# Performance work log

Hardware: AMD Instinct MI355X
Metric: run time of the kernel (lower is better)

The kernel has to match this reference:

```python
import jax, jax.numpy as jnp
import numpy as np

PI = 3.141592653589793
DET_THRESHOLD = 0.25
MAX_DET = 100
REG_HEAD = 4
DEPTH_MEAN = 28.01  # smoke_coder.depth_ref[0]
DIM_REF = (3.88, 1.63, 1.53)  # smoke_coder.dim_ref[0] (l, h, w)


def setup_inputs() -> dict:
    key = jax.random.key(0)
    k1, k2, k3, k4 = jax.random.split(key, 4)
    B, C, H, W = 32, 3, 256, 832  # stride-4 feature map of 3328x1024 images
    pred_heatmap = jax.random.uniform(k1, (B, C, H, W), dtype=jnp.float32)
    pred_regression = jax.random.normal(k2, (B, C + 1, H, W), dtype=jnp.float32) * 0.1  # REG_HEAD=4 channels
    trans_mat = jnp.tile(jnp.array([[0.25, 0.0, 0.0], [0.0, 0.25, 0.0], [0.0, 0.0, 1.0]], jnp.float32), (B, 1, 1))
    K_mat = jnp.tile(jnp.array([[2100.0, 0.0, 1664.0], [0.0, 2100.0, 512.0], [0.0, 0.0, 1.0]], jnp.float32), (B, 1, 1))
    size = jnp.tile(jnp.array([3328.0, 1024.0], jnp.float32), (B, 1))  # (img_w, img_h)
    h_cam = jax.random.uniform(k3, (B,), jnp.float32, 1.4, 2.0)
    dimensions = jax.random.uniform(k4, (B, 3), jnp.float32, 1.5, 4.0)
    return dict(pred_heatmap=pred_heatmap, pred_regression=pred_regression, trans_mat=trans_mat,
                K_mat=K_mat, size=size, h_cam=h_cam, dimensions=dimensions)


def reference(pred_heatmap, pred_regression, trans_mat, K_mat, size, h_cam, dimensions):
    B, C, H, W = pred_heatmap.shape
    K = MAX_DET
    # ---- nms_hm: 3x3 max-pool, keep local maxima ----
    hmax = jax.lax.reduce_window(pred_heatmap, -jnp.inf, jax.lax.max, (1, 1, 3, 3), (1, 1, 1, 1), 'SAME')
    heat = pred_heatmap * (hmax == pred_heatmap).astype(pred_heatmap.dtype)
    # ---- select_topk: per-class topk then global topk ----
    scores_c, inds_c = jax.lax.top_k(heat.reshape(B, C, H * W), K)  # [B,C,K]
    ys_c = (inds_c // W).astype(jnp.float32)
    xs_c = (inds_c % W).astype(jnp.float32)
    scores, topk_ind = jax.lax.top_k(scores_c.reshape(B, C * K), K)  # [B,K]
    clses = (topk_ind // K).astype(jnp.float32)
    inds = jnp.take_along_axis(inds_c.reshape(B, C * K), topk_ind, axis=1)
    ys = jnp.take_along_axis(ys_c.reshape(B, C * K), topk_ind, axis=1)
    xs = jnp.take_along_axis(xs_c.reshape(B, C * K), topk_ind, axis=1)
    feat = pred_regression.reshape(B, REG_HEAD, H * W).transpose(0, 2, 1)  # [B,HW,R]
    pois = jnp.take_along_axis(feat, inds[:, :, None], axis=1).reshape(-1, REG_HEAD)  # [B*K,R]
    log_dv_delta = pois[:, 0]
    off_u = pois[:, 1]
    ori = pois[:, 2:]
    # ---- feature points -> image points via inverse affine ----
    pts = jnp.stack([xs.reshape(-1), ys.reshape(-1)], axis=1)
    pts = pts + jnp.stack([off_u, jnp.zeros_like(off_u)], axis=1)
    pts_h = jnp.concatenate([pts, jnp.ones((pts.shape[0], 1), pts.dtype)], axis=1)  # [N,3]
    obj = jnp.repeat(jnp.arange(B), K)
    trans_inv = jnp.linalg.inv(trans_mat)[obj]  # [N,3,3]
    img_pts = jnp.einsum('nij,nj->ni', trans_inv, pts_h)[:, :2]
    # ---- per-object camera params ----
    Ks = K_mat[obj]
    h = h_cam[obj]
    kd = dimensions[obj]
    fx, fy, cx = Ks[:, 0, 0], Ks[:, 1, 1], Ks[:, 0, 2]
    dim_ref = jnp.array(DIM_REF, jnp.float32)
    dims = jnp.where(jnp.isfinite(kd), kd, dim_ref[None, :])
    # ---- geometric depth decode ----
    h_ref = h - dims[:, 1] / 2.0
    log_dv_ref = jnp.log(jnp.clip(fy * jnp.abs(h_ref), 1e-7, None) / DEPTH_MEAN)
    log_dv = jnp.clip(log_dv_ref + log_dv_delta, -4.0, 8.0)
    depths = jnp.clip(fy * jnp.abs(h_ref) * jnp.exp(-log_dv), 0.5, 120.0)
    px = (img_pts[:, 0] - cx) * depths / fx
    locs = jnp.stack([px, h, depths], axis=1)  # [N,3]
    # ---- decode_orientation (SMOKE) ----
    rays = jnp.arctan(locs[:, 0] / (locs[:, 2] + 1e-7))
    alphas = jnp.arctan(ori[:, 0] / (ori[:, 1] + 1e-7))
    alphas = alphas + jnp.where(ori[:, 1] >= 0, -PI / 2, PI / 2)
    rotys = alphas + rays
    rotys = jnp.where(rotys > PI, rotys - 2 * PI, rotys)
    rotys = jnp.where(rotys < -PI, rotys + 2 * PI, rotys)
    # ---- encode_box2d: build 3D corners, rotate, project, clamp ----
    cos, sin = jnp.cos(rotys), jnp.sin(rotys)
    cx8 = jnp.array([-0.5, 0.5, 0.5, 0.5, 0.5, -0.5, -0.5, -0.5], jnp.float32)
    cy8 = jnp.array([-1.0, -1.0, 0.0, 0.0, -1.0, -1.0, 0.0, 0.0], jnp.float32)
    cz8 = jnp.array([-0.5, -0.5, -0.5, 0.5, 0.5, 0.5, 0.5, -0.5], jnp.float32)
    xc = dims[:, 0:1] * cx8  # l
    yc = dims[:, 1:2] * cy8  # h
    zc = dims[:, 2:3] * cz8  # w
    bx = cos[:, None] * xc + sin[:, None] * zc
    bz = -sin[:, None] * xc + cos[:, None] * zc
    box3d = jnp.stack([bx, yc, bz], axis=1) + locs[:, :, None]  # [N,3,8]
    proj = jnp.einsum('nij,njk->nik', Ks, box3d)
    uv = proj[:, :2, :] / proj[:, 2:3, :]
    img_w = size.reshape(-1)[0]
    img_h = size.reshape(-1)[1]
    xmins = jnp.clip(jnp.min(uv[:, 0, :], axis=1), 0.0, img_w)
    xmaxs = jnp.clip(jnp.max(uv[:, 0, :], axis=1), 0.0, img_w)
    ymins = jnp.clip(jnp.min(uv[:, 1, :], axis=1), 0.0, img_h)
    ymaxs = jnp.clip(jnp.max(uv[:, 1, :], axis=1), 0.0, img_h)
    box2d = jnp.stack([xmins, ymins, xmaxs, ymaxs], axis=1)
    pred_dims = jnp.roll(dims, -1, axis=1)  # (l,h,w)->(h,w,l)
    result = jnp.concatenate([clses.reshape(-1, 1), alphas[:, None], box2d, pred_dims, locs,
                              rotys[:, None], scores.reshape(-1, 1)], axis=1)  # [N,14]
    # fixed-shape equivalent of boolean filtering: zero out rows below threshold
    keep = (result[:, -1] > DET_THRESHOLD).astype(result.dtype)
    return result * keep[:, None]
```

## Files before the change

kernel.cpp:

```cpp
#include <hip/hip_runtime.h>
#include <math.h>

#define B_ 32
#define C_ 3
#define H_ 256
#define W_ 832
#define HW_ (H_*W_)
#define NQ (W_/4)
#define K_ 100
#define RPB 16
#define PARTS (H_/RPB)
#define BLK 256
#define CAP 2048
#define NB 2048
#define TIE_CAP 128
#define SEL_PASSES 6
#define QPW 62
#define SLOTS 384
#define T_HOT 0.982f
#define NCAND2 (C_*PARTS*SLOTS)

typedef unsigned long long ull;

template<int N>
__device__ inline void bitonic_sort_desc(ull* s) {
    for (int k = 2; k <= N; k <<= 1) {
        for (int j = k >> 1; j > 0; j >>= 1) {
            __syncthreads();
            for (int i = threadIdx.x; i < N; i += BLK) {
                int ixj = i ^ j;
                if (ixj > i) {
                    ull a = s[i], b = s[ixj];
                    bool up = ((i & k) == 0);
                    if (up ? (a < b) : (a > b)) { s[i] = b; s[ixj] = a; }
                }
            }
        }
    }
    __syncthreads();
}

__device__ inline void find_digit(const unsigned* __restrict__ hist,
                                  unsigned* __restrict__ wtot,
                                  const int kneed,
                                  int* __restrict__ d_s,
                                  int* __restrict__ krem_s,
                                  int* __restrict__ m_s) {
    const int tid = threadIdx.x;
    const int lane = tid & 63;
    const int wid = tid >> 6;
    unsigned l[8];
    unsigned Ls = 0;
    #pragma unroll
    for (int j = 0; j < 8; ++j) { l[j] = hist[tid * 8 + j]; Ls += l[j]; }
    unsigned x = Ls;
    #pragma unroll
    for (int off = 1; off < 64; off <<= 1) {
        unsigned y = __shfl_down(x, off);
        if (lane + off < 64) x += y;
    }
    if (lane == 0) wtot[wid] = x;
    __syncthreads();
    unsigned tail = 0;
    #pragma unroll
    for (int w = 0; w < 4; ++w) if (w > wid) tail += wtot[w];
    unsigned s = x - Ls + tail;
    #pragma unroll
    for (int j = 7; j >= 0; --j) {
        const unsigned Sj = s + l[j];
        if (Sj >= (unsigned)kneed && s < (unsigned)kneed) {
            *d_s = tid * 8 + j;
            *krem_s = kneed - (int)s;
            *m_s = (int)l[j];
        }
        s = Sj;
    }
    __syncthreads();
}

__device__ inline void select_topk(const ull* __restrict__ buf, const int cnt,
                                   ull* __restrict__ dst,
                                   unsigned* __restrict__ hist,
                                   ull* __restrict__ tie,
                                   unsigned* __restrict__ wtot,
                                   int* __restrict__ sh) {
    const int tid = threadIdx.x;
    const int lane = tid & 63;
    if (tid == 0) sh[0] = 0;
    int kneed = K_;
    int pshift = 0;
    ull prefix = 0;
    for (int pass = 0; pass < SEL_PASSES; ++pass) {
        const int rs = 53 - 11 * pass;
        const int shift = (rs > 0) ? rs : 0;
        #pragma unroll
        for (int j = 0; j < NB / BLK; ++j) hist[tid + j * BLK] = 0u;
        if (tid == 0) sh[1] = 0;
        __syncthreads();
        if (pass == 0) {
            for (int i = tid; i < cnt; i += BLK) {
                const unsigned dg = (unsigned)(buf[i] >> shift) & 2047u;
                ull unclaimed = __ballot(1);
                while (unclaimed) {
                    const int leader = __ffsll((long long)unclaimed) - 1;
                    const unsigned ldg = __shfl(dg, leader);
                    const ull same = __ballot(dg == ldg);
                    if (lane == leader)
                        atomicAdd(&hist[ldg], (unsigned)__popcll(same));
                    unclaimed &= ~same;
                }
            }
        } else {
            for (int i = tid; i < cnt; i += BLK) {
                const ull key = buf[i];
                if ((key >> pshift) != prefix) continue;
                atomicAdd(&hist[(unsigned)(key >> shift) & 2047u], 1u);
            }
        }
        __syncthreads();
        find_digit(hist, wtot, kneed, &sh[2], &sh[3], &sh[4]);
        const int d = sh[2], krem = sh[3], m = sh[4];
        const bool last = (m <= TIE_CAP) || (pass == SEL_PASSES - 1);
        for (int i = tid; i < cnt; i += BLK) {
            const ull key = buf[i];
            if (pass > 0 && (key >> pshift) != prefix) continue;
            const int dg = (int)((unsigned)(key >> shift) & 2047u);
            if (dg > d) {
                dst[atomicAdd(&sh[0], 1)] = key;
            } else if (last && dg == d) {
                const int p = atomicAdd(&sh[1], 1);
                if (p < TIE_CAP) tie[p] = key;
            }
        }
        __syncthreads();
        if (last) {
            const int n1 = K_ - krem;
            if (sh[1] <= TIE_CAP) {
                const int mm = sh[1];
                for (int i = tid; i < mm; i += BLK) {
                    const ull key = tie[i];
                    int r = 0;
                    for (int j = 0; j < mm; ++j) r += (tie[j] > key) ? 1 : 0;
                    if (r < krem) dst[n1 + r] = key;
                }
            } else {
                for (int i = tid; i < krem; i += BLK) dst[n1 + i] = tie[0];
            }
            __syncthreads();
            return;
        }
        prefix = (prefix << 11) | (ull)(unsigned)d;
        pshift = shift;
        kneed = krem;
    }
}

__device__ inline void select_topk_g(const ull* __restrict__ A, const int cnt,
                                     ull* __restrict__ dst,
                                     unsigned* __restrict__ hist,
                                     ull* __restrict__ tie,
                                     unsigned* __restrict__ wtot,
                                     int* __restrict__ sh) {
    const int tid = threadIdx.x;
    const int lane = tid & 63;
    if (tid == 0) sh[0] = 0;
    int kneed = K_;
    int pshift = 0;
    ull prefix = 0;
    for (int pass = 0; pass < SEL_PASSES; ++pass) {
        const int rs = 53 - 11 * pass;
        const int shift = (rs > 0) ? rs : 0;
        #pragma unroll
        for (int j = 0; j < NB / BLK; ++j) hist[tid + j * BLK] = 0u;
        if (tid == 0) sh[1] = 0;
        __syncthreads();
        if (pass == 0) {
            for (int i = tid; i < cnt; i += BLK) {
                const unsigned dg = (unsigned)(A[i] >> shift) & 2047u;
                ull unclaimed = __ballot(1);
                while (unclaimed) {
                    const int leader = __ffsll((long long)unclaimed) - 1;
                    const unsigned ldg = __shfl(dg, leader);
                    const ull same = __ballot(dg == ldg);
                    if (lane == leader)
                        atomicAdd(&hist[ldg], (unsigned)__popcll(same));
                    unclaimed &= ~same;
                }
            }
        } else {
            for (int i = tid; i < cnt; i += BLK) {
                const ull key = A[i];
                if ((key >> pshift) != prefix) continue;
                atomicAdd(&hist[(unsigned)(key >> shift) & 2047u], 1u);
            }
        }
        __syncthreads();
        find_digit(hist, wtot, kneed, &sh[2], &sh[3], &sh[4]);
        const int d = sh[2], krem = sh[3], m = sh[4];
        const bool last = (m <= TIE_CAP) || (pass == SEL_PASSES - 1);
        for (int i = tid; i < cnt; i += BLK) {
            const ull key = A[i];
            if (pass > 0 && (key >> pshift) != prefix) continue;
            const int dg = (int)((unsigned)(key >> shift) & 2047u);
            if (dg > d) {
                dst[atomicAdd(&sh[0], 1)] = key;
            } else if (last && dg == d) {
                const int p = atomicAdd(&sh[1], 1);
                if (p < TIE_CAP) tie[p] = key;
            }
        }
        __syncthreads();
        if (last) {
            const int n1 = K_ - krem;
            if (sh[1] <= TIE_CAP) {
                const int mm = sh[1];
                for (int i = tid; i < mm; i += BLK) {
                    const ull key = tie[i];
                    int r = 0;
                    for (int j = 0; j < mm; ++j) r += (tie[j] > key) ? 1 : 0;
                    if (r < krem) dst[n1 + r] = key;
                }
            } else {
                for (int i = tid; i < krem; i += BLK) dst[n1 + i] = tie[0];
            }
            __syncthreads();
            return;
        }
        prefix = (prefix << 11) | (ull)(unsigned)d;
        pshift = shift;
        kneed = krem;
    }
}

__global__ void __launch_bounds__(BLK) topk_part_kernel(
        const float* __restrict__ heat, ull* __restrict__ parts2) {
    const int chan = blockIdx.x / PARTS;
    const int c    = chan % C_;
    const int part = blockIdx.x % PARTS;
    const float* __restrict__ hp = heat + (size_t)chan * HW_;
    const int r0 = part * RPB;
    const int tid = threadIdx.x;
    const int lane = tid & 63;
    const int wid = tid >> 6;

    const int q = QPW * wid + lane - 1;
    const bool ghost = (q < 0) || (q >= NQ);
    const int qc = (q < 0) ? 0 : ((q >= NQ) ? NQ - 1 : q);
    const bool emitter = (lane >= 1) && (lane <= QPW) && !ghost;

    __shared__ ull sbuf[CAP];
    __shared__ unsigned hist[NB];
    __shared__ ull tie[TIE_CAP];
    __shared__ unsigned wtot[4];
    __shared__ int scnt, nhot, wpos;
    __shared__ int selsh[5];
    if (tid == 0) { scnt = 0; nhot = 0; wpos = 0; }

    float4 R[6];
    #pragma unroll
    for (int j = 0; j < 6; ++j) {
        int row = r0 - 1 + j;
        row = (row < 0) ? 0 : ((row > H_ - 1) ? H_ - 1 : row);
        R[j] = reinterpret_cast<const float4*>(hp + (size_t)row * W_)[qc];
    }
    __syncthreads();

    #pragma unroll
    for (int r = 0; r < RPB; ++r) {
        const int y = r0 + r;
        const float4 ra = R[r % 6];
        const float4 rb = R[(r + 1) % 6];
        const float4 rc = R[(r + 2) % 6];
        if (r < RPB - 4) {
            const int yn = (y + 5 > H_ - 1) ? H_ - 1 : y + 5;
            R[r % 6] = reinterpret_cast<const float4*>(hp + (size_t)yn * W_)[qc];
        }

        float4 vm;
        vm.x = fmaxf(fmaxf(ra.x, rb.x), rc.x);
        vm.y = fmaxf(fmaxf(ra.y, rb.y), rc.y);
        vm.z = fmaxf(fmaxf(ra.z, rb.z), rc.z);
        vm.w = fmaxf(fmaxf(ra.w, rb.w), rc.w);
        if (ghost) { vm.x = vm.y = vm.z = vm.w = -INFINITY; }

        const float left  = __shfl_up(vm.w, 1);
        const float right = __shfl_down(vm.x, 1);

        const float vn[6] = {left, vm.x, vm.y, vm.z, vm.w, right};
        const float vv[4] = {rb.x, rb.y, rb.z, rb.w};
        ull m[4];
        bool pk[4];
        #pragma unroll
        for (int i = 0; i < 4; ++i) {
            pk[i] = emitter && (vv[i] >= vn[i]) && (vv[i] >= vn[i+1]) && (vv[i] >= vn[i+2]);
            m[i] = __ballot(pk[i]);
        }
        const int tot = (int)(__popcll(m[0]) + __popcll(m[1]) +
                              __popcll(m[2]) + __popcll(m[3]));
        if (tot) {
            int base = 0;
            if (lane == 0) base = atomicAdd(&scnt, tot);
            base = __shfl(base, 0);
            int off = 0;
            #pragma unroll
            for (int i = 0; i < 4; ++i) {
                if (pk[i]) {
                    const unsigned p = (unsigned)(y * W_ + q * 4 + i);
                    const unsigned tiek = ((unsigned)c << 18) | p;
                    const ull key = ((ull)__float_as_uint(vv[i]) << 32) | (ull)(~tiek);
                    const int rank = (int)__popcll(m[i] & ((1ULL << lane) - 1ULL));
                    const int pos = base + off + rank;
                    if (pos < CAP) sbuf[pos] = key;
                }
                off += (int)__popcll(m[i]);
            }
        }
    }
    __syncthreads();

    const int cc = (scnt < CAP) ? scnt : CAP;
    ull* o = parts2 + (size_t)blockIdx.x * SLOTS;

    if (cc <= K_) {
        for (int i = tid; i < cc; i += BLK) o[i] = sbuf[i];
        for (int i = cc + tid; i < SLOTS; i += BLK) o[i] = 0ULL;
        return;
    }

    for (int i0 = wid * 64; i0 < cc; i0 += BLK) {
        const int i = i0 + lane;
        bool hotf = false;
        if (i < cc) hotf = (__uint_as_float((unsigned)(sbuf[i] >> 32)) >= T_HOT);
        const ull mh = __ballot(hotf);
        if (lane == 0 && mh) atomicAdd(&nhot, (int)__popcll(mh));
    }
    __syncthreads();
    const int nh = nhot;

    if (nh >= K_ && nh <= SLOTS) {
        for (int i0 = wid * 64; i0 < cc; i0 += BLK) {
            const int i = i0 + lane;
            ull key = 0ULL; bool hotf = false;
            if (i < cc) {
                key = sbuf[i];
                hotf = (__uint_as_float((unsigned)(key >> 32)) >= T_HOT);
            }
            const ull mh = __ballot(hotf);
            int basep = 0;
            if (lane == 0 && mh) basep = atomicAdd(&wpos, (int)__popcll(mh));
            basep = __shfl(basep, 0);
            if (hotf) o[basep + (int)__popcll(mh & ((1ULL << lane) - 1ULL))] = key;
        }
        for (int i = nh + tid; i < SLOTS; i += BLK) o[i] = 0ULL;
    } else {
        select_topk(sbuf, cc, o, hist, tie, wtot, selsh);
        for (int i = K_ + tid; i < SLOTS; i += BLK) o[i] = 0ULL;
    }
}

__global__ void __launch_bounds__(BLK) merge_geom_kernel(
        const ull* __restrict__ parts2, const float* __restrict__ reg,
        const float* __restrict__ trans, const float* __restrict__ Km,
        const float* __restrict__ sz, const float* __restrict__ hcam,
        const float* __restrict__ dimen, float* __restrict__ out) {
    const int b = blockIdx.x;
    const int tid = threadIdx.x;
    __shared__ unsigned hist[NB];
    __shared__ ull sel[128];
    __shared__ ull tie[TIE_CAP];
    __shared__ unsigned wtot[4];
    __shared__ int selsh[5];

    const ull* src = parts2 + (size_t)b * NCAND2;

    if (tid < 128) sel[tid] = 0ULL;
    __syncthreads();

    select_topk_g(src, NCAND2, sel, hist, tie, wtot, selsh);

    bitonic_sort_desc<128>(sel);

    for (int i = tid; i < K_; i += BLK) {
        const ull key = sel[i];
        const unsigned tiek = ~(unsigned)(key & 0xFFFFFFFFULL);
        const float score = __uint_as_float((unsigned)(key >> 32));
        const float clsf = (float)((tiek >> 18) & 3u);
        unsigned hw = tiek & 0x3FFFFu;
        if (hw >= HW_) hw = 0;
        const float xs = (float)(hw % W_);
        const float ys = (float)(hw / W_);

        const float* rg = reg + (size_t)b * 4 * HW_;
        const float delta = rg[hw];
        const float off_u = rg[HW_ + hw];
        const float ori0  = rg[2 * HW_ + hw];
        const float ori1  = rg[3 * HW_ + hw];

        const float* T = trans + b * 9;
        const float t00=T[0], t01=T[1], t02=T[2], t10=T[3], t11=T[4], t12=T[5],
                    t20=T[6], t21=T[7], t22=T[8];
        const float det3 = t00*(t11*t22 - t12*t21) - t01*(t10*t22 - t12*t20)
                         + t02*(t10*t21 - t11*t20);
        const float idt = 1.0f / det3;
        const float i00 = (t11*t22 - t12*t21)*idt;
        const float i01 = (t02*t21 - t01*t22)*idt;
        const float i02 = (t01*t12 - t02*t11)*idt;

        const float pu = xs + off_u;
        const float img_x = i00*pu + i01*ys + i02;

        const float* Kb = Km + b * 9;
        const float k00=Kb[0],k01=Kb[1],k02=Kb[2],k10=Kb[3],k11=Kb[4],k12=Kb[5],
                    k20=Kb[6],k21=Kb[7],k22=Kb[8];
        const float fx = k00, fy = k11, cx = k02;
        const float h = hcam[b];
        float d0 = dimen[b*3+0], d1 = dimen[b*3+1], d2 = dimen[b*3+2];
        if (!isfinite(d0)) d0 = 3.88f;
        if (!isfinite(d1)) d1 = 1.63f;
        if (!isfinite(d2)) d2 = 1.53f;

        const float h_ref = h - d1 * 0.5f;
        const float fyh = fy * fabsf(h_ref);
        const float log_dv_ref = logf(fmaxf(fyh, 1e-7f) / 28.01f);
        const float log_dv = fminf(fmaxf(log_dv_ref + delta, -4.0f), 8.0f);
        const float depth = fminf(fmaxf(fyh * expf(-log_dv), 0.5f), 120.0f);
        const float px = (img_x - cx) * depth / fx;

        const float PI_F  = 3.14159265358979323846f;
        const float ray = atanf(px / (depth + 1e-7f));
        float alpha = atanf(ori0 / (ori1 + 1e-7f));
        alpha += (ori1 >= 0.0f) ? -1.5707963267948966f : 1.5707963267948966f;
        float roty = alpha + ray;
        if (roty >  PI_F) roty -= 6.283185307179586f;
        if (roty < -PI_F) roty += 6.283185307179586f;

        const float cosr = cosf(roty), sinr = sinf(roty);
        const float cx8[8] = {-0.5f, 0.5f, 0.5f, 0.5f, 0.5f,-0.5f,-0.5f,-0.5f};
        const float cy8[8] = {-1.0f,-1.0f, 0.0f, 0.0f,-1.0f,-1.0f, 0.0f, 0.0f};
        const float cz8[8] = {-0.5f,-0.5f,-0.5f, 0.5f, 0.5f, 0.5f, 0.5f,-0.5f};
        float umin = 1e30f, umax = -1e30f, vmin = 1e30f, vmax = -1e30f;
        #pragma unroll
        for (int j = 0; j < 8; ++j) {
            const float xc = d0 * cx8[j];
            const float yc = d1 * cy8[j];
            const float zc = d2 * cz8[j];
            const float X = cosr*xc + sinr*zc + px;
            const float Y = yc + h;
            const float Z = -sinr*xc + cosr*zc + depth;
            const float w = k20*X + k21*Y + k22*Z;
            const float u = (k00*X + k01*Y + k02*Z) / w;
            const float v = (k10*X + k11*Y + k12*Z) / w;
            umin = fminf(umin, u); umax = fmaxf(umax, u);
            vmin = fminf(vmin, v); vmax = fmaxf(vmax, v);
        }
        const float img_w = sz[0], img_h = sz[1];
        const float xmin = fminf(fmaxf(umin, 0.0f), img_w);
        const float xmax = fminf(fmaxf(umax, 0.0f), img_w);
        const float ymin = fminf(fmaxf(vmin, 0.0f), img_h);
        const float ymax = fminf(fmaxf(vmax, 0.0f), img_h);

        const float keep = (score > 0.25f) ? 1.0f : 0.0f;
        float* o = out + (size_t)(b * K_ + i) * 14;
        o[0]  = clsf  * keep;
        o[1]  = alpha * keep;
        o[2]  = xmin  * keep;
        o[3]  = ymin  * keep;
        o[4]  = xmax  * keep;
        o[5]  = ymax  * keep;
        o[6]  = d1    * keep;
        o[7]  = d2    * keep;
        o[8]  = d0    * keep;
        o[9]  = px    * keep;
        o[10] = h     * keep;
        o[11] = depth * keep;
        o[12] = roty  * keep;
        o[13] = score * keep;
    }
}

extern "C" void kernel_launch(void* const* d_in, const int* in_sizes, int n_in,
                              void* d_out, int out_size, void* d_ws, size_t ws_size,
                              hipStream_t stream) {
    const float* heat  = (const float*)d_in[0];
    const float* reg   = (const float*)d_in[1];
    const float* trans = (const float*)d_in[2];
    const float* Kmat  = (const float*)d_in[3];
    const float* sz    = (const float*)d_in[4];
    const float* hcam  = (const float*)d_in[5];
    const float* dimen = (const float*)d_in[6];
    float* out = (float*)d_out;

    ull* parts2 = (ull*)d_ws;

    topk_part_kernel<<<B_ * C_ * PARTS, BLK, 0, stream>>>(heat, parts2);
    merge_geom_kernel<<<B_, BLK, 0, stream>>>(
        parts2, reg, trans, Kmat, sz, hcam, dimen, out);
}
```

Baseline: 278.8 us.

## Split candidates into two score tiers and merge only the hot tier

Each partition block now sorts its local-maximum candidates into two tiers, a very-hot tier (>=0.9995) and a warm tier, and writes them to separate slabs together with a packed per-partition count. The merge kernel reads the counts, prefix-sums them and compacts only the hot-tier candidates into shared memory. When those guarantee at least K entries it runs the select on that small buffer instead of a radix select over every partition slot. Otherwise it falls back to the full global select over the larger slabs. The aim is to cut the per-batch merge work in the serial second kernel, at the cost of extra ballots and atomics in the partition kernel and more workspace writes.

```diff
diff --git a/kernel.cpp b/kernel.cpp
--- a/kernel.cpp
+++ b/kernel.cpp
@@ -16,9 +16,12 @@
 #define TIE_CAP 128
 #define SEL_PASSES 6
 #define QPW 62
-#define SLOTS 384
-#define T_HOT 0.982f
-#define NCAND2 (C_*PARTS*SLOTS)
+#define SA 128
+#define SB 512
+#define T_A 0.9995f
+#define T_B 0.982f
+#define PPB (C_*PARTS)
+#define SLAB (SA+SB)
 
 typedef unsigned long long ull;
 
@@ -233,7 +236,8 @@
 }
 
 __global__ void __launch_bounds__(BLK) topk_part_kernel(
-        const float* __restrict__ heat, ull* __restrict__ parts2) {
+        const float* __restrict__ heat, ull* __restrict__ parts2,
+        unsigned* __restrict__ cnts) {
     const int chan = blockIdx.x / PARTS;
     const int c    = chan % C_;
     const int part = blockIdx.x % PARTS;
@@ -252,9 +256,9 @@
     __shared__ unsigned hist[NB];
     __shared__ ull tie[TIE_CAP];
     __shared__ unsigned wtot[4];
-    __shared__ int scnt, nhot, wpos;
+    __shared__ int scnt, nA, nB, wpA, wpB;
     __shared__ int selsh[5];
-    if (tid == 0) { scnt = 0; nhot = 0; wpos = 0; }
+    if (tid == 0) { scnt = 0; nA = 0; nB = 0; wpA = 0; wpB = 0; }
 
     float4 R[6];
     #pragma unroll
@@ -319,64 +323,114 @@
     __syncthreads();
 
     const int cc = (scnt < CAP) ? scnt : CAP;
-    ull* o = parts2 + (size_t)blockIdx.x * SLOTS;
-
-    if (cc <= K_) {
-        for (int i = tid; i < cc; i += BLK) o[i] = sbuf[i];
-        for (int i = cc + tid; i < SLOTS; i += BLK) o[i] = 0ULL;
-        return;
-    }
+    ull* oA = parts2 + (size_t)blockIdx.x * SLAB;
+    ull* oB = oA + SA;
 
     for (int i0 = wid * 64; i0 < cc; i0 += BLK) {
         const int i = i0 + lane;
-        bool hotf = false;
-        if (i < cc) hotf = (__uint_as_float((unsigned)(sbuf[i] >> 32)) >= T_HOT);
-        const ull mh = __ballot(hotf);
-        if (lane == 0 && mh) atomicAdd(&nhot, (int)__popcll(mh));
-    }
-    __syncthreads();
-    const int nh = nhot;
-
-    if (nh >= K_ && nh <= SLOTS) {
+        float v = -1.f;
+        if (i < cc) v = __uint_as_float((unsigned)(sbuf[i] >> 32));
+        const ull ma = __ballot(v >= T_A);
+        const ull mb = __ballot(v >= T_B && v < T_A);
+        if (lane == 0) {
+            if (ma) atomicAdd(&nA, (int)__popcll(ma));
+            if (mb) atomicAdd(&nB, (int)__popcll(mb));
+        }
+    }
+    __syncthreads();
+    const int nhA = nA, nhB = nB;
+    const bool fb = (nhA > SA) || (nhB > SB) ||
+                    ((nhA + nhB) < K_ && (nhA + nhB) < cc);
+
+    int cntA, gA, cntB;
+    if (cc <= K_) {
+        for (int i = tid; i < cc; i += BLK) oA[i] = sbuf[i];
+        for (int i = cc + tid; i < SA; i += BLK) oA[i] = 0ULL;
+        for (int i = tid; i < SB; i += BLK) oB[i] = 0ULL;
+        cntA = cc; gA = (nhA < cc) ? nhA : cc; cntB = 0;
+    } else if (!fb) {
         for (int i0 = wid * 64; i0 < cc; i0 += BLK) {
             const int i = i0 + lane;
-            ull key = 0ULL; bool hotf = false;
-            if (i < cc) {
-                key = sbuf[i];
-                hotf = (__uint_as_float((unsigned)(key >> 32)) >= T_HOT);
-            }
-            const ull mh = __ballot(hotf);
-            int basep = 0;
-            if (lane == 0 && mh) basep = atomicAdd(&wpos, (int)__popcll(mh));
-            basep = __shfl(basep, 0);
-            if (hotf) o[basep + (int)__popcll(mh & ((1ULL << lane) - 1ULL))] = key;
-        }
-        for (int i = nh + tid; i < SLOTS; i += BLK) o[i] = 0ULL;
+            ull key = 0ULL; float v = -1.f;
+            if (i < cc) { key = sbuf[i]; v = __uint_as_float((unsigned)(key >> 32)); }
+            const bool fa  = (v >= T_A);
+            const bool fbb = (v >= T_B) && (v < T_A);
+            const ull ma = __ballot(fa);
+            const ull mb = __ballot(fbb);
+            int ba = 0, bb = 0;
+            if (lane == 0) {
+                if (ma) ba = atomicAdd(&wpA, (int)__popcll(ma));
+                if (mb) bb = atomicAdd(&wpB, (int)__popcll(mb));
+            }
+            ba = __shfl(ba, 0); bb = __shfl(bb, 0);
+            if (fa)  oA[ba + (int)__popcll(ma & ((1ULL << lane) - 1ULL))] = key;
+            if (fbb) oB[bb + (int)__popcll(mb & ((1ULL << lane) - 1ULL))] = key;
+        }
+        for (int i = nhA + tid; i < SA; i += BLK) oA[i] = 0ULL;
+        for (int i = nhB + tid; i < SB; i += BLK) oB[i] = 0ULL;
+        cntA = nhA; gA = nhA; cntB = nhB;
     } else {
-        select_topk(sbuf, cc, o, hist, tie, wtot, selsh);
-        for (int i = K_ + tid; i < SLOTS; i += BLK) o[i] = 0ULL;
-    }
+        select_topk(sbuf, cc, oA, hist, tie, wtot, selsh);
+        for (int i = K_ + tid; i < SA; i += BLK) oA[i] = 0ULL;
+        for (int i = tid; i < SB; i += BLK) oB[i] = 0ULL;
+        cntA = K_; gA = (nhA < K_) ? nhA : K_; cntB = 0;
+    }
+    if (tid == 0)
+        cnts[blockIdx.x] = (unsigned)cntA | ((unsigned)gA << 8) |
+                           ((unsigned)cntB << 16);
 }
 
 __global__ void __launch_bounds__(BLK) merge_geom_kernel(
-        const ull* __restrict__ parts2, const float* __restrict__ reg,
+        const ull* __restrict__ parts2, const unsigned* __restrict__ cnts,
+        const float* __restrict__ reg,
         const float* __restrict__ trans, const float* __restrict__ Km,
         const float* __restrict__ sz, const float* __restrict__ hcam,
         const float* __restrict__ dimen, float* __restrict__ out) {
     const int b = blockIdx.x;
     const int tid = threadIdx.x;
+    __shared__ ull buf[CAP];
     __shared__ unsigned hist[NB];
     __shared__ ull sel[128];
     __shared__ ull tie[TIE_CAP];
     __shared__ unsigned wtot[4];
     __shared__ int selsh[5];
-
-    const ull* src = parts2 + (size_t)b * NCAND2;
-
+    __shared__ int cA[PPB], gAsh[PPB], offA[PPB + 1];
+    __shared__ int gsum_s;
+
+    const int p0 = b * PPB;
+    if (tid < PPB) {
+        const unsigned w = cnts[p0 + tid];
+        cA[tid]  = (int)(w & 255u);
+        gAsh[tid] = (int)((w >> 8) & 255u);
+    }
     if (tid < 128) sel[tid] = 0ULL;
     __syncthreads();
-
-    select_topk_g(src, NCAND2, sel, hist, tie, wtot, selsh);
+    if (tid == 0) {
+        int acc = 0, g = 0;
+        for (int j = 0; j < PPB; ++j) { offA[j] = acc; acc += cA[j]; g += gAsh[j]; }
+        offA[PPB] = acc; gsum_s = g;
+    }
+    __syncthreads();
+    const int ntot = offA[PPB];
+    const int gsum = gsum_s;
+
+    if (gsum >= K_ && ntot <= CAP) {
+        for (int t = tid; t < ntot; t += BLK) {
+            int j = 0;
+            while (offA[j + 1] <= t) ++j;
+            buf[t] = parts2[(size_t)(p0 + j) * SLAB + (t - offA[j])];
+        }
+        __syncthreads();
+        if (ntot <= K_) {
+            for (int i = tid; i < ntot; i += BLK) sel[i] = buf[i];
+            __syncthreads();
+        } else {
+            select_topk(buf, ntot, sel, hist, tie, wtot, selsh);
+        }
+    } else {
+        select_topk_g(parts2 + (size_t)p0 * SLAB, PPB * SLAB,
+                      sel, hist, tie, wtot, selsh);
+    }
 
     bitonic_sort_desc<128>(sel);
 
@@ -490,9 +544,12 @@
     const float* dimen = (const float*)d_in[6];
     float* out = (float*)d_out;
 
-    ull* parts2 = (ull*)d_ws;
-
-    topk_part_kernel<<<B_ * C_ * PARTS, BLK, 0, stream>>>(heat, parts2);
+    char* ws = (char*)d_ws;
+    ull* parts2 = (ull*)ws;
+    ws += (size_t)B_ * PPB * SLAB * sizeof(ull);
+    unsigned* cnts = (unsigned*)ws;
+
+    topk_part_kernel<<<B_ * C_ * PARTS, BLK, 0, stream>>>(heat, parts2, cnts);
     merge_geom_kernel<<<B_, BLK, 0, stream>>>(
-        parts2, reg, trans, Kmat, sz, hcam, dimen, out);
-}
+        parts2, cnts, reg, trans, Kmat, sz, hcam, dimen, out);
+}
```

After: 223.2 us (median of 2 runs). -19.9%, faster.
